# Kernel tuning notes

Measured on AMD Instinct MI355X. Metric: run time of the kernel, lower is better.

## Reference

```python
import jax, jax.numpy as jnp
import numpy as np

EMBED_DIM = 512
NUM_HEADS = 8
HEAD_DIM = EMBED_DIM // NUM_HEADS
LOCAL_SIZE = 17
NUM_WTOK = 64
SCALING = float(HEAD_DIM) ** -0.5


def get_overlap_segments(x, window_size):
    # x: (BH, T, D) -> (BH, T, W, D); centered zero-padded sliding windows
    if window_size % 2 == 0:
        window_size += 1
    pad = (window_size - 1) // 2
    xp = jnp.pad(x, ((0, 0), (pad, pad), (0, 0)))
    idx = jnp.arange(x.shape[1])[:, None] + jnp.arange(window_size)[None, :]
    return xp[:, idx, :]


def setup_inputs() -> dict:
    key = jax.random.key(0)
    k = jax.random.split(key, 5)
    B, T, E = 2, NUM_WTOK + 4096, EMBED_DIM
    s = 1.0 / np.sqrt(E).astype(np.float32)
    return {
        "x": jax.random.normal(k[0], (B, T, E), jnp.float32),
        "W_qkv": jax.random.normal(k[1], (E, 3 * E), jnp.float32) * s,
        "b_qkv": jax.random.normal(k[2], (3 * E,), jnp.float32) * 0.01,
        "W_out": jax.random.normal(k[3], (E, E), jnp.float32) * s,
        "b_out": jax.random.normal(k[4], (E,), jnp.float32) * 0.01,
    }


def reference(x, W_qkv, b_qkv, W_out, b_out):
    b, t, E = x.shape
    H, Dh, NW = NUM_HEADS, HEAD_DIM, NUM_WTOK
    BH = b * H
    qkv = x @ W_qkv + b_qkv
    Q, K, V = jnp.split(qkv, 3, axis=-1)
    Q = Q * SCALING

    def heads(z):  # (b,t,E) -> (b*H, t, Dh)
        return z.reshape(b, t, H, Dh).transpose(0, 2, 1, 3).reshape(BH, t, Dh)

    Q, K, V = heads(Q), heads(K), heads(V)
    Qw, Qf = Q[:, :NW], Q[:, NW:]
    Kw, Kf = K[:, :NW], K[:, NW:]
    Vw, Vf = V[:, :NW], V[:, NW:]
    t_fea = t - NW
    pad_len = (NW - t_fea % NW) % NW
    Kp = jnp.pad(Kf, ((0, 0), (0, pad_len), (0, 0)))
    Vp = jnp.pad(Vf, ((0, 0), (0, pad_len), (0, 0)))
    chunk = (t_fea + pad_len) // NW
    Kp = Kp.reshape(BH, NW, chunk, Dh)
    Vp = Vp.reshape(BH, NW, chunk, Dh)

    # ---- word-token stream: each wtok attends to its own key + its feature chunk
    Kcat = jnp.concatenate([Kw[:, :, None, :], Kp], axis=2)  # (BH, NW, 1+chunk, Dh)
    Vcat = jnp.concatenate([Vw[:, :, None, :], Vp], axis=2)
    aw = jax.nn.softmax(jnp.einsum('bnd,bncd->bnc', Qw, Kcat), axis=-1)
    out_wtok = jnp.einsum('bnc,bncd->bnd', aw, Vcat)  # (BH, NW, Dh)

    # broadcast each wtok output over its chunk of feature positions
    out_wtok_expa = jnp.repeat(out_wtok, chunk, axis=1)[:, :t_fea]  # (BH, t_fea, Dh)

    # ---- feature stream: local windowed attention + global wtok token
    Kseg = get_overlap_segments(Kf, LOCAL_SIZE)  # (BH, t_fea, W, Dh)
    Vseg = get_overlap_segments(Vf, LOCAL_SIZE)
    Kfull = jnp.concatenate([out_wtok_expa[:, :, None, :], Kseg], axis=2)
    scores = jnp.einsum('btd,btwd->btw', Qf, Kfull)  # (BH, t_fea, 1+W)

    w_wtok = scores[:, :, 0]  # (BH, t_fea)
    w_wtok = jnp.pad(w_wtok, ((0, 0), (0, pad_len)), constant_values=-jnp.inf)
    w_wtok = jax.nn.softmax(w_wtok.reshape(BH, NW, chunk), axis=-1)
    w_wtok = w_wtok.reshape(BH, NW * chunk)[:, :t_fea, None]
    w_fea = jax.nn.softmax(scores[:, :, 1:], axis=-1)
    attn = jnp.concatenate([w_wtok, w_fea], axis=-1)  # (BH, t_fea, 1+W)

    Vfull = jnp.concatenate([out_wtok_expa[:, :, None, :], Vseg], axis=2)
    out_fea = jnp.einsum('btw,btwd->btd', attn, Vfull)  # (BH, t_fea, Dh)

    out = jnp.concatenate([out_wtok, out_fea], axis=1)  # (BH, t, Dh)
    out = out.reshape(b, H, t, Dh).transpose(0, 2, 1, 3).reshape(b, t, E)
    return out @ W_out + b_out
```

## Files before the change

### kernel.cpp

```cpp
#include <hip/hip_runtime.h>
#include <hip/hip_bf16.h>
#include <math.h>

#define T_TOT 4160
#define H_N   8
#define NWTOK 64
#define TFEA  4096

typedef __bf16 bf16x8 __attribute__((ext_vector_type(8)));
typedef float  f32x4  __attribute__((ext_vector_type(4)));

__device__ inline ushort f2b(float f) {
  __hip_bfloat16 h = __float2bfloat16(f);
  return *reinterpret_cast<ushort*>(&h);
}
__device__ inline float b2f(ushort u) {
  union { uint i; float v; } a;
  a.i = ((uint)u) << 16;
  return a.v;
}
__device__ inline uint pk2(float a, float b) {
  return (uint)f2b(a) | ((uint)f2b(b) << 16);
}
__device__ inline void unpack8(uint4 u, float* f) {
  union { uint i; float v; } a;
  a.i = u.x << 16;        f[0] = a.v;
  a.i = u.x & 0xffff0000u; f[1] = a.v;
  a.i = u.y << 16;        f[2] = a.v;
  a.i = u.y & 0xffff0000u; f[3] = a.v;
  a.i = u.z << 16;        f[4] = a.v;
  a.i = u.z & 0xffff0000u; f[5] = a.v;
  a.i = u.w << 16;        f[6] = a.v;
  a.i = u.w & 0xffff0000u; f[7] = a.v;
}

__global__ __launch_bounds__(256) void conv_x(
    const float* __restrict__ X, ushort* __restrict__ Xb, int n8) {
  const int i = blockIdx.x * 256 + threadIdx.x;
  if (i >= n8) return;
  const float4 a = reinterpret_cast<const float4*>(X)[i * 2];
  const float4 b = reinterpret_cast<const float4*>(X)[i * 2 + 1];
  union { ushort u[8]; uint4 v; } r;
  r.u[0] = f2b(a.x); r.u[1] = f2b(a.y); r.u[2] = f2b(a.z); r.u[3] = f2b(a.w);
  r.u[4] = f2b(b.x); r.u[5] = f2b(b.y); r.u[6] = f2b(b.z); r.u[7] = f2b(b.w);
  reinterpret_cast<uint4*>(Xb)[i] = r.v;
}

__global__ __launch_bounds__(256) void conv_w2(
    const float* __restrict__ W0, ushort* __restrict__ WT0,
    const float* __restrict__ W1, ushort* __restrict__ WT1) {
  const int z = blockIdx.z;
  if (z == 1 && blockIdx.y >= 8) return;
  const float* __restrict__ W = z ? W1 : W0;
  ushort* __restrict__ WT = z ? WT1 : WT0;
  const int C = z ? 512 : 1536;
  __shared__ float tile[64][65];
  const int r0 = blockIdx.x * 64, c0 = blockIdx.y * 64;
  const int tid = threadIdx.x;
  const int rr = tid >> 4, c4 = (tid & 15) * 4;
#pragma unroll
  for (int q = 0; q < 4; ++q) {
    const int r = q * 16 + rr;
    const float4 v = *reinterpret_cast<const float4*>(&W[(size_t)(r0 + r) * C + c0 + c4]);
    tile[r][c4] = v.x; tile[r][c4 + 1] = v.y; tile[r][c4 + 2] = v.z; tile[r][c4 + 3] = v.w;
  }
  __syncthreads();
#pragma unroll
  for (int q = 0; q < 4; ++q) {
    const int cr = q * 16 + rr;
    ushort4 o;
    o.x = f2b(tile[c4][cr]);
    o.y = f2b(tile[c4 + 1][cr]);
    o.z = f2b(tile[c4 + 2][cr]);
    o.w = f2b(tile[c4 + 3][cr]);
    *reinterpret_cast<ushort4*>(&WT[(size_t)(c0 + cr) * 512 + r0 + c4]) = o;
  }
}

template<int MODE>
__global__ __launch_bounds__(256) void gemm_mfma(
    const ushort* __restrict__ A, const ushort* __restrict__ BT,
    const float* __restrict__ bias, void* __restrict__ O0v,
    void* __restrict__ O1v, void* __restrict__ O2v) {
  __shared__ ushort sA[128 * 64];
  __shared__ ushort sB[128 * 64];
  const int tid = threadIdx.x;
  const int lane = tid & 63, wave = tid >> 6;
  const int m0 = blockIdx.x * 128, n0 = blockIdx.y * 128;
  const int wm = wave >> 1, wn = wave & 1;

  f32x4 acc[4][4] = {};

  auto stage = [&](int kt) {
    const ushort* Ag = A + (size_t)m0 * 512 + kt * 64;
    const ushort* Bg = BT + (size_t)n0 * 512 + kt * 64;
#pragma unroll
    for (int r = 0; r < 4; ++r) {
      const int rowbase = r * 32 + wave * 8;
      const int row = rowbase + (lane >> 3);
      const int c = lane & 7;
      const int cc = c ^ (row & 7);
      __builtin_amdgcn_global_load_lds(
          (const __attribute__((address_space(1))) void*)(Ag + (size_t)row * 512 + cc * 8),
          (__attribute__((address_space(3))) void*)(sA + rowbase * 64), 16, 0, 0);
      __builtin_amdgcn_global_load_lds(
          (const __attribute__((address_space(1))) void*)(Bg + (size_t)row * 512 + cc * 8),
          (__attribute__((address_space(3))) void*)(sB + rowbase * 64), 16, 0, 0);
    }
  };

  stage(0);
  for (int kt = 0; kt < 8; ++kt) {
    __syncthreads();
#pragma unroll
    for (int ks = 0; ks < 2; ++ks) {
      bf16x8 af[4], bfr[4];
      const int cc = ks * 4 + (lane >> 4);
      const int rA = wm * 64 + (lane & 15);
      const int rB = wn * 64 + (lane & 15);
#pragma unroll
      for (int i = 0; i < 4; ++i) {
        const int ra = rA + i * 16;
        af[i] = *reinterpret_cast<const bf16x8*>(&sA[ra * 64 + ((cc ^ (ra & 7)) << 3)]);
        const int rb = rB + i * 16;
        bfr[i] = *reinterpret_cast<const bf16x8*>(&sB[rb * 64 + ((cc ^ (rb & 7)) << 3)]);
      }
#pragma unroll
      for (int i = 0; i < 4; ++i)
#pragma unroll
        for (int j = 0; j < 4; ++j)
          acc[i][j] = __builtin_amdgcn_mfma_f32_16x16x32_bf16(af[i], bfr[j], acc[i][j], 0, 0, 0);
    }
    __syncthreads();
    if (kt < 7) stage(kt + 1);
  }

#pragma unroll
  for (int i = 0; i < 4; ++i) {
#pragma unroll
    for (int j = 0; j < 4; ++j) {
      const f32x4 a = acc[i][j];
      const int n = n0 + wn * 64 + j * 16 + (lane & 15);
      const float bv = bias[n];
#pragma unroll
      for (int r = 0; r < 4; ++r) {
        const int m = m0 + wm * 64 + i * 16 + ((lane >> 4) << 2) + r;
        const float v = a[r] + bv;
        if (MODE == 0) {
          const int bb = m / T_TOT, t = m - bb * T_TOT;
          const int which = n >> 9, e = n & 511;
          const int h = e >> 6, d = e & 63;
          const size_t idx = ((size_t)(bb * H_N + h) * T_TOT + t) * 64 + d;
          if (which == 0)      ((ushort*)O0v)[idx] = f2b(v * 0.125f);
          else if (which == 1) ((ushort*)O1v)[idx] = f2b(v);
          else                 ((ushort*)O2v)[idx] = f2b(v);
        } else {
          ((float*)O0v)[(size_t)m * 512 + n] = v;
        }
      }
    }
  }
}

__global__ __launch_bounds__(256) void fused_attn(
    const ushort* __restrict__ Qb, const ushort* __restrict__ Kb,
    const ushort* __restrict__ Vb, ushort* __restrict__ AObf) {
  const int bh = blockIdx.x >> 6;
  const int n  = blockIdx.x & 63;
  const int tid = threadIdx.x;
  const int t  = tid & 63;
  const int wv = tid >> 6;
  __shared__ ushort Ks[80 * 64];
  __shared__ ushort Vs[80 * 64];
  __shared__ ushort kwr[64];
  __shared__ ushort vwr[64];
  __shared__ float qw[64];
  __shared__ float ow[64];
  __shared__ float ps[4][18][64];
  const size_t base = (size_t)bh * T_TOT * 64;
  const int tok0 = n * 64;

#pragma unroll
  for (int it = 0; it < 3; ++it) {
    const int u = it * 256 + tid;
    if (u < 640) {
      const int r = u >> 3, c16 = u & 7;
      const int tok = tok0 - 8 + r;
      uint4 kv = make_uint4(0, 0, 0, 0), vv = make_uint4(0, 0, 0, 0);
      if (tok >= 0 && tok < TFEA) {
        kv = *reinterpret_cast<const uint4*>(&Kb[base + (size_t)(NWTOK + tok) * 64 + c16 * 8]);
        vv = *reinterpret_cast<const uint4*>(&Vb[base + (size_t)(NWTOK + tok) * 64 + c16 * 8]);
      }
      const int sw = (c16 ^ (r & 7)) << 3;
      *reinterpret_cast<uint4*>(&Ks[r * 64 + sw]) = kv;
      *reinterpret_cast<uint4*>(&Vs[r * 64 + sw]) = vv;
    }
  }
  if (tid < 8)
    *reinterpret_cast<uint4*>(&kwr[tid * 8]) =
        *reinterpret_cast<const uint4*>(&Kb[base + n * 64 + tid * 8]);
  else if (tid < 16)
    *reinterpret_cast<uint4*>(&vwr[(tid - 8) * 8]) =
        *reinterpret_cast<const uint4*>(&Vb[base + n * 64 + (tid - 8) * 8]);
  else if (tid < 32) {
    const int j = tid - 16;
    const ushort4 u = *reinterpret_cast<const ushort4*>(&Qb[base + n * 64 + j * 4]);
    qw[j * 4 + 0] = b2f(u.x); qw[j * 4 + 1] = b2f(u.y);
    qw[j * 4 + 2] = b2f(u.z); qw[j * 4 + 3] = b2f(u.w);
  }

  float q[16];
  {
    const ushort* qr = &Qb[base + (size_t)(NWTOK + tok0 + t) * 64 + wv * 16];
#pragma unroll
    for (int h8 = 0; h8 < 2; ++h8) {
      const uint4 u4 = *reinterpret_cast<const uint4*>(&qr[h8 * 8]);
      unpack8(u4, &q[h8 * 8]);
    }
  }
  __syncthreads();

  float aw_l, aw0;
  {
    const int row = t + 8, r7 = row & 7;
    float acc = 0.f, acc0 = 0.f;
#pragma unroll
    for (int g = 0; g < 8; ++g) {
      float f[8], f0[8];
      const uint4 u  = *reinterpret_cast<const uint4*>(&Ks[row * 64 + ((g ^ r7) << 3)]);
      const uint4 u0 = *reinterpret_cast<const uint4*>(&kwr[g * 8]);
      unpack8(u, f); unpack8(u0, f0);
#pragma unroll
      for (int k = 0; k < 8; ++k) {
        const float qv = qw[g * 8 + k];
        acc  += qv * f[k];
        acc0 += qv * f0[k];
      }
    }
    float mx = fmaxf(acc, acc0);
#pragma unroll
    for (int off = 32; off >= 1; off >>= 1) mx = fmaxf(mx, __shfl_xor(mx, off));
    const float e = __expf(acc - mx), e0 = __expf(acc0 - mx);
    float sum = e;
#pragma unroll
    for (int off = 32; off >= 1; off >>= 1) sum += __shfl_xor(sum, off);
    sum += e0;
    aw_l = e / sum;
    aw0  = e0 / sum;
  }
  {
    float pv[16];
    const int row = t + 8, r7 = row & 7;
    const float a0 = (t == 0) ? aw0 : 0.f;
#pragma unroll
    for (int hb = 0; hb < 2; ++hb) {
      const int g = wv * 2 + hb;
      float f[8], f0[8];
      const uint4 u  = *reinterpret_cast<const uint4*>(&Vs[row * 64 + ((g ^ r7) << 3)]);
      const uint4 u0 = *reinterpret_cast<const uint4*>(&vwr[g * 8]);
      unpack8(u, f); unpack8(u0, f0);
#pragma unroll
      for (int k = 0; k < 8; ++k) pv[hb * 8 + k] = aw_l * f[k] + a0 * f0[k];
    }
#pragma unroll
    for (int off = 1; off < 64; off <<= 1)
#pragma unroll
      for (int k = 0; k < 16; ++k) pv[k] += __shfl_xor(pv[k], off);
    if (t == 0) {
#pragma unroll
      for (int k = 0; k < 16; ++k) ow[wv * 16 + k] = pv[k];
      uint4 s1, s2;
      s1.x = pk2(pv[0], pv[1]);   s1.y = pk2(pv[2], pv[3]);
      s1.z = pk2(pv[4], pv[5]);   s1.w = pk2(pv[6], pv[7]);
      s2.x = pk2(pv[8], pv[9]);   s2.y = pk2(pv[10], pv[11]);
      s2.z = pk2(pv[12], pv[13]); s2.w = pk2(pv[14], pv[15]);
      ushort* orow = &AObf[((size_t)(bh >> 3) * T_TOT + n) * 512 + (bh & 7) * 64 + wv * 16];
      *reinterpret_cast<uint4*>(&orow[0]) = s1;
      *reinterpret_cast<uint4*>(&orow[8]) = s2;
    }
  }
  __syncthreads();

  const int d0a = wv * 2, d0b = wv * 2 + 1;
#pragma unroll
  for (int w = 0; w < 17; ++w) {
    const int r = t + w, rx = r & 7;
    float f[16];
    const uint4 ua = *reinterpret_cast<const uint4*>(&Ks[r * 64 + ((d0a ^ rx) << 3)]);
    const uint4 ub = *reinterpret_cast<const uint4*>(&Ks[r * 64 + ((d0b ^ rx) << 3)]);
    unpack8(ua, f); unpack8(ub, f + 8);
    float acc = 0.f;
#pragma unroll
    for (int k = 0; k < 16; ++k) acc += q[k] * f[k];
    ps[wv][w][t] = acc;
  }
  {
    float acc = 0.f;
#pragma unroll
    for (int k = 0; k < 16; ++k) acc += q[k] * ow[wv * 16 + k];
    ps[wv][17][t] = acc;
  }
  __syncthreads();

  float s[17];
#pragma unroll
  for (int w = 0; w < 17; ++w)
    s[w] = ps[0][w][t] + ps[1][w][t] + ps[2][w][t] + ps[3][w][t];
  float s0 = ps[0][17][t] + ps[1][17][t] + ps[2][17][t] + ps[3][17][t];

  float m = s[0];
#pragma unroll
  for (int w = 1; w < 17; ++w) m = fmaxf(m, s[w]);
  float sum = 0.f;
#pragma unroll
  for (int w = 0; w < 17; ++w) { s[w] = __expf(s[w] - m); sum += s[w]; }
  const float inv = 1.f / sum;
#pragma unroll
  for (int w = 0; w < 17; ++w) s[w] *= inv;

  float mx = s0;
#pragma unroll
  for (int off = 32; off >= 1; off >>= 1) mx = fmaxf(mx, __shfl_xor(mx, off));
  const float e0 = __expf(s0 - mx);
  float es = e0;
#pragma unroll
  for (int off = 32; off >= 1; off >>= 1) es += __shfl_xor(es, off);
  const float w0 = e0 / es;

  const int bb = bh >> 3, h = bh & 7;
  ushort* orow = &AObf[((size_t)bb * T_TOT + NWTOK + tok0 + t) * 512 + h * 64 + wv * 16];
#pragma unroll
  for (int hb = 0; hb < 2; ++hb) {
    const int d0 = wv * 2 + hb;
    float o[8];
#pragma unroll
    for (int k = 0; k < 8; ++k) o[k] = w0 * ow[d0 * 8 + k];
#pragma unroll
    for (int w = 0; w < 17; ++w) {
      const int r = t + w, rx = r & 7;
      const uint4 u4 = *reinterpret_cast<const uint4*>(&Vs[r * 64 + ((d0 ^ rx) << 3)]);
      float f[8]; unpack8(u4, f);
#pragma unroll
      for (int k = 0; k < 8; ++k) o[k] += s[w] * f[k];
    }
    uint4 st;
    st.x = pk2(o[0], o[1]); st.y = pk2(o[2], o[3]);
    st.z = pk2(o[4], o[5]); st.w = pk2(o[6], o[7]);
    *reinterpret_cast<uint4*>(&orow[hb * 8]) = st;
  }
}

extern "C" void kernel_launch(void* const* d_in, const int* in_sizes, int n_in,
                              void* d_out, int out_size, void* d_ws, size_t ws_size,
                              hipStream_t stream) {
  const float* x    = (const float*)d_in[0];
  const float* Wqkv = (const float*)d_in[1];
  const float* bqkv = (const float*)d_in[2];
  const float* Wout = (const float*)d_in[3];
  const float* bout = (const float*)d_in[4];
  float* out = (float*)d_out;

  const size_t SZ = (size_t)16 * T_TOT * 64;
  ushort* Qb = (ushort*)d_ws;
  ushort* Kb = Qb + SZ;
  ushort* Vb = Kb + SZ;
  ushort* Xb    = Vb + SZ;
  ushort* WqkvT = Xb + SZ;
  ushort* WoutT = WqkvT + (size_t)1536 * 512;
  ushort* AObf  = WoutT + (size_t)512 * 512;

  conv_x<<<2080, 256, 0, stream>>>(x, Xb, (int)(SZ / 8));
  conv_w2<<<dim3(8, 24, 2), 256, 0, stream>>>(Wqkv, WqkvT, Wout, WoutT);
  gemm_mfma<0><<<dim3(65, 12), 256, 0, stream>>>(Xb, WqkvT, bqkv, Qb, Kb, Vb);
  fused_attn<<<1024, 256, 0, stream>>>(Qb, Kb, Vb, AObf);
  gemm_mfma<1><<<dim3(65, 4), 256, 0, stream>>>(AObf, WoutT, bout, out, nullptr, nullptr);
}
```

Before: 142.9 us.

## Compute local window scores with MFMA and shrink output GEMM tile width

The local-window QK scores in the attention kernel are now computed with bf16 MFMA as a 64x80 block score matrix held in LDS, replacing per-thread scalar dot products with cross-wave partial-sum reduction. K and V share one LDS buffer: V is prefetched into registers while the softmax runs, then written over K. The output projection GEMM uses a 64-wide N tile, doubling its grid to raise occupancy on the small GEMM. The trade-offs are redundant MFMA work on keys outside each query's window, an extra barrier, and more LDS for the fp32 score matrix.

Result: no change. 142.6 us (-0.2%).

```diff
diff --git a/kernel.cpp b/kernel.cpp
--- a/kernel.cpp
+++ b/kernel.cpp
@@ -82,14 +82,17 @@
     const ushort* __restrict__ A, const ushort* __restrict__ BT,
     const float* __restrict__ bias, void* __restrict__ O0v,
     void* __restrict__ O1v, void* __restrict__ O2v) {
+  constexpr int BN = (MODE == 0) ? 128 : 64;
+  constexpr int WN = BN / 2;
+  constexpr int NJ = WN / 16;
   __shared__ ushort sA[128 * 64];
-  __shared__ ushort sB[128 * 64];
+  __shared__ ushort sB[BN * 64];
   const int tid = threadIdx.x;
   const int lane = tid & 63, wave = tid >> 6;
-  const int m0 = blockIdx.x * 128, n0 = blockIdx.y * 128;
+  const int m0 = blockIdx.x * 128, n0 = blockIdx.y * BN;
   const int wm = wave >> 1, wn = wave & 1;
 
-  f32x4 acc[4][4] = {};
+  f32x4 acc[4][NJ] = {};
 
   auto stage = [&](int kt) {
     const ushort* Ag = A + (size_t)m0 * 512 + kt * 64;
@@ -103,9 +106,10 @@
       __builtin_amdgcn_global_load_lds(
           (const __attribute__((address_space(1))) void*)(Ag + (size_t)row * 512 + cc * 8),
           (__attribute__((address_space(3))) void*)(sA + rowbase * 64), 16, 0, 0);
-      __builtin_amdgcn_global_load_lds(
-          (const __attribute__((address_space(1))) void*)(Bg + (size_t)row * 512 + cc * 8),
-          (__attribute__((address_space(3))) void*)(sB + rowbase * 64), 16, 0, 0);
+      if (r < BN / 32)
+        __builtin_amdgcn_global_load_lds(
+            (const __attribute__((address_space(1))) void*)(Bg + (size_t)row * 512 + cc * 8),
+            (__attribute__((address_space(3))) void*)(sB + rowbase * 64), 16, 0, 0);
     }
   };
 
@@ -114,21 +118,23 @@
     __syncthreads();
 #pragma unroll
     for (int ks = 0; ks < 2; ++ks) {
-      bf16x8 af[4], bfr[4];
+      bf16x8 af[4], bfr[NJ];
       const int cc = ks * 4 + (lane >> 4);
       const int rA = wm * 64 + (lane & 15);
-      const int rB = wn * 64 + (lane & 15);
 #pragma unroll
       for (int i = 0; i < 4; ++i) {
         const int ra = rA + i * 16;
         af[i] = *reinterpret_cast<const bf16x8*>(&sA[ra * 64 + ((cc ^ (ra & 7)) << 3)]);
-        const int rb = rB + i * 16;
-        bfr[i] = *reinterpret_cast<const bf16x8*>(&sB[rb * 64 + ((cc ^ (rb & 7)) << 3)]);
       }
 #pragma unroll
+      for (int j = 0; j < NJ; ++j) {
+        const int rb = wn * WN + j * 16 + (lane & 15);
+        bfr[j] = *reinterpret_cast<const bf16x8*>(&sB[rb * 64 + ((cc ^ (rb & 7)) << 3)]);
+      }
+#pragma unroll
       for (int i = 0; i < 4; ++i)
 #pragma unroll
-        for (int j = 0; j < 4; ++j)
+        for (int j = 0; j < NJ; ++j)
           acc[i][j] = __builtin_amdgcn_mfma_f32_16x16x32_bf16(af[i], bfr[j], acc[i][j], 0, 0, 0);
     }
     __syncthreads();
@@ -138,9 +144,9 @@
 #pragma unroll
   for (int i = 0; i < 4; ++i) {
 #pragma unroll
-    for (int j = 0; j < 4; ++j) {
+    for (int j = 0; j < NJ; ++j) {
       const f32x4 a = acc[i][j];
-      const int n = n0 + wn * 64 + j * 16 + (lane & 15);
+      const int n = n0 + wn * WN + j * 16 + (lane & 15);
       const float bv = bias[n];
 #pragma unroll
       for (int r = 0; r < 4; ++r) {
@@ -170,13 +176,13 @@
   const int tid = threadIdx.x;
   const int t  = tid & 63;
   const int wv = tid >> 6;
-  __shared__ ushort Ks[80 * 64];
-  __shared__ ushort Vs[80 * 64];
+  __shared__ ushort KV[80 * 64];
+  __shared__ float  S[64 * 80];
   __shared__ ushort kwr[64];
   __shared__ ushort vwr[64];
   __shared__ float qw[64];
   __shared__ float ow[64];
-  __shared__ float ps[4][18][64];
+  __shared__ float ps0[4][64];
   const size_t base = (size_t)bh * T_TOT * 64;
   const int tok0 = n * 64;
 
@@ -186,14 +192,10 @@
     if (u < 640) {
       const int r = u >> 3, c16 = u & 7;
       const int tok = tok0 - 8 + r;
-      uint4 kv = make_uint4(0, 0, 0, 0), vv = make_uint4(0, 0, 0, 0);
-      if (tok >= 0 && tok < TFEA) {
+      uint4 kv = make_uint4(0, 0, 0, 0);
+      if (tok >= 0 && tok < TFEA)
         kv = *reinterpret_cast<const uint4*>(&Kb[base + (size_t)(NWTOK + tok) * 64 + c16 * 8]);
-        vv = *reinterpret_cast<const uint4*>(&Vb[base + (size_t)(NWTOK + tok) * 64 + c16 * 8]);
-      }
-      const int sw = (c16 ^ (r & 7)) << 3;
-      *reinterpret_cast<uint4*>(&Ks[r * 64 + sw]) = kv;
-      *reinterpret_cast<uint4*>(&Vs[r * 64 + sw]) = vv;
+      *reinterpret_cast<uint4*>(&KV[r * 64 + ((c16 ^ (r & 7)) << 3)]) = kv;
     }
   }
   if (tid < 8)
@@ -208,16 +210,6 @@
     qw[j * 4 + 0] = b2f(u.x); qw[j * 4 + 1] = b2f(u.y);
     qw[j * 4 + 2] = b2f(u.z); qw[j * 4 + 3] = b2f(u.w);
   }
-
-  float q[16];
-  {
-    const ushort* qr = &Qb[base + (size_t)(NWTOK + tok0 + t) * 64 + wv * 16];
-#pragma unroll
-    for (int h8 = 0; h8 < 2; ++h8) {
-      const uint4 u4 = *reinterpret_cast<const uint4*>(&qr[h8 * 8]);
-      unpack8(u4, &q[h8 * 8]);
-    }
-  }
   __syncthreads();
 
   float aw_l, aw0;
@@ -227,7 +219,7 @@
 #pragma unroll
     for (int g = 0; g < 8; ++g) {
       float f[8], f0[8];
-      const uint4 u  = *reinterpret_cast<const uint4*>(&Ks[row * 64 + ((g ^ r7) << 3)]);
+      const uint4 u  = *reinterpret_cast<const uint4*>(&KV[row * 64 + ((g ^ r7) << 3)]);
       const uint4 u0 = *reinterpret_cast<const uint4*>(&kwr[g * 8]);
       unpack8(u, f); unpack8(u0, f0);
 #pragma unroll
@@ -248,6 +240,74 @@
     aw_l = e / sum;
     aw0  = e0 / sum;
   }
+
+  {
+    f32x4 accs[5] = {};
+#pragma unroll
+    for (int kt = 0; kt < 2; ++kt) {
+      const bf16x8 a = *reinterpret_cast<const bf16x8*>(
+          &Qb[base + (size_t)(NWTOK + tok0 + wv * 16 + (t & 15)) * 64 +
+              kt * 32 + ((t >> 4) << 3)]);
+#pragma unroll
+      for (int j = 0; j < 5; ++j) {
+        const int key = j * 16 + (t & 15);
+        const int koff8 = kt * 4 + (t >> 4);
+        const bf16x8 b = *reinterpret_cast<const bf16x8*>(
+            &KV[key * 64 + ((koff8 ^ (key & 7)) << 3)]);
+        accs[j] = __builtin_amdgcn_mfma_f32_16x16x32_bf16(a, b, accs[j], 0, 0, 0);
+      }
+    }
+#pragma unroll
+    for (int j = 0; j < 5; ++j)
+#pragma unroll
+      for (int r = 0; r < 4; ++r)
+        S[(wv * 16 + ((t >> 4) << 2) + r) * 80 + j * 16 + (t & 15)] = accs[j][r];
+  }
+  __syncthreads();
+
+  uint4 vreg0 = make_uint4(0, 0, 0, 0), vreg1 = vreg0, vreg2 = vreg0;
+  {
+    const int u0 = tid, u1 = 256 + tid, u2 = 512 + tid;
+    { const int r = u0 >> 3, c16 = u0 & 7, tok = tok0 - 8 + r;
+      if (tok >= 0 && tok < TFEA)
+        vreg0 = *reinterpret_cast<const uint4*>(&Vb[base + (size_t)(NWTOK + tok) * 64 + c16 * 8]); }
+    { const int r = u1 >> 3, c16 = u1 & 7, tok = tok0 - 8 + r;
+      if (tok >= 0 && tok < TFEA)
+        vreg1 = *reinterpret_cast<const uint4*>(&Vb[base + (size_t)(NWTOK + tok) * 64 + c16 * 8]); }
+    if (u2 < 640) {
+      const int r = u2 >> 3, c16 = u2 & 7, tok = tok0 - 8 + r;
+      if (tok >= 0 && tok < TFEA)
+        vreg2 = *reinterpret_cast<const uint4*>(&Vb[base + (size_t)(NWTOK + tok) * 64 + c16 * 8]);
+    }
+  }
+
+  float s[17];
+  {
+    const float* Srow = &S[t * 80];
+    float m = -1e30f;
+#pragma unroll
+    for (int w = 0; w < 17; ++w) { s[w] = Srow[t + w]; m = fmaxf(m, s[w]); }
+    float sum = 0.f;
+#pragma unroll
+    for (int w = 0; w < 17; ++w) { s[w] = __expf(s[w] - m); sum += s[w]; }
+    const float inv = 1.f / sum;
+#pragma unroll
+    for (int w = 0; w < 17; ++w) s[w] *= inv;
+  }
+
+  {
+    const int u0 = tid, u1 = 256 + tid, u2 = 512 + tid;
+    { const int r = u0 >> 3, c16 = u0 & 7;
+      *reinterpret_cast<uint4*>(&KV[r * 64 + ((c16 ^ (r & 7)) << 3)]) = vreg0; }
+    { const int r = u1 >> 3, c16 = u1 & 7;
+      *reinterpret_cast<uint4*>(&KV[r * 64 + ((c16 ^ (r & 7)) << 3)]) = vreg1; }
+    if (u2 < 640) {
+      const int r = u2 >> 3, c16 = u2 & 7;
+      *reinterpret_cast<uint4*>(&KV[r * 64 + ((c16 ^ (r & 7)) << 3)]) = vreg2;
+    }
+  }
+  __syncthreads();
+
   {
     float pv[16];
     const int row = t + 8, r7 = row & 7;
@@ -256,7 +316,7 @@
     for (int hb = 0; hb < 2; ++hb) {
       const int g = wv * 2 + hb;
       float f[8], f0[8];
-      const uint4 u  = *reinterpret_cast<const uint4*>(&Vs[row * 64 + ((g ^ r7) << 3)]);
+      const uint4 u  = *reinterpret_cast<const uint4*>(&KV[row * 64 + ((g ^ r7) << 3)]);
       const uint4 u0 = *reinterpret_cast<const uint4*>(&vwr[g * 8]);
       unpack8(u, f); unpack8(u0, f0);
 #pragma unroll
@@ -281,43 +341,22 @@
   }
   __syncthreads();
 
-  const int d0a = wv * 2, d0b = wv * 2 + 1;
-#pragma unroll
-  for (int w = 0; w < 17; ++w) {
-    const int r = t + w, rx = r & 7;
-    float f[16];
-    const uint4 ua = *reinterpret_cast<const uint4*>(&Ks[r * 64 + ((d0a ^ rx) << 3)]);
-    const uint4 ub = *reinterpret_cast<const uint4*>(&Ks[r * 64 + ((d0b ^ rx) << 3)]);
-    unpack8(ua, f); unpack8(ub, f + 8);
+  {
+    float q[16];
+    const ushort* qr = &Qb[base + (size_t)(NWTOK + tok0 + t) * 64 + wv * 16];
+#pragma unroll
+    for (int h8 = 0; h8 < 2; ++h8) {
+      const uint4 u4 = *reinterpret_cast<const uint4*>(&qr[h8 * 8]);
+      unpack8(u4, &q[h8 * 8]);
+    }
     float acc = 0.f;
 #pragma unroll
-    for (int k = 0; k < 16; ++k) acc += q[k] * f[k];
-    ps[wv][w][t] = acc;
-  }
-  {
-    float acc = 0.f;
-#pragma unroll
     for (int k = 0; k < 16; ++k) acc += q[k] * ow[wv * 16 + k];
-    ps[wv][17][t] = acc;
-  }
-  __syncthreads();
-
-  float s[17];
-#pragma unroll
-  for (int w = 0; w < 17; ++w)
-    s[w] = ps[0][w][t] + ps[1][w][t] + ps[2][w][t] + ps[3][w][t];
-  float s0 = ps[0][17][t] + ps[1][17][t] + ps[2][17][t] + ps[3][17][t];
-
-  float m = s[0];
-#pragma unroll
-  for (int w = 1; w < 17; ++w) m = fmaxf(m, s[w]);
-  float sum = 0.f;
-#pragma unroll
-  for (int w = 0; w < 17; ++w) { s[w] = __expf(s[w] - m); sum += s[w]; }
-  const float inv = 1.f / sum;
-#pragma unroll
-  for (int w = 0; w < 17; ++w) s[w] *= inv;
-
+    ps0[wv][t] = acc;
+  }
+  __syncthreads();
+
+  float s0 = ps0[0][t] + ps0[1][t] + ps0[2][t] + ps0[3][t];
   float mx = s0;
 #pragma unroll
   for (int off = 32; off >= 1; off >>= 1) mx = fmaxf(mx, __shfl_xor(mx, off));
@@ -338,7 +377,7 @@
 #pragma unroll
     for (int w = 0; w < 17; ++w) {
       const int r = t + w, rx = r & 7;
-      const uint4 u4 = *reinterpret_cast<const uint4*>(&Vs[r * 64 + ((d0 ^ rx) << 3)]);
+      const uint4 u4 = *reinterpret_cast<const uint4*>(&KV[r * 64 + ((d0 ^ rx) << 3)]);
       float f[8]; unpack8(u4, f);
 #pragma unroll
       for (int k = 0; k < 8; ++k) o[k] += s[w] * f[k];
@@ -373,5 +412,5 @@
   conv_w2<<<dim3(8, 24, 2), 256, 0, stream>>>(Wqkv, WqkvT, Wout, WoutT);
   gemm_mfma<0><<<dim3(65, 12), 256, 0, stream>>>(Xb, WqkvT, bqkv, Qb, Kb, Vb);
   fused_attn<<<1024, 256, 0, stream>>>(Qb, Kb, Vb, AObf);
-  gemm_mfma<1><<<dim3(65, 4), 256, 0, stream>>>(AObf, WoutT, bout, out, nullptr, nullptr);
-}
+  gemm_mfma<1><<<dim3(65, 8), 256, 0, stream>>>(AObf, WoutT, bout, out, nullptr, nullptr);
+}
```
